# Optimization experiments

Hardware: AMD Instinct MI355X
Metric: run time of the kernel (lower is better)

## Reference

```python
import jax, jax.numpy as jnp
import numpy as np

BATCH = 1048576
IN_DIM = 64   # input_dim = A.shape[1]
OUT_DIM = 16  # output_dim = A.shape[0]


def setup_inputs() -> dict:
    key = jax.random.key(0)
    k1, k2, k3 = jax.random.split(key, 3)
    y = jax.random.normal(k1, (BATCH, IN_DIM), dtype=jnp.float32)
    A = jax.random.normal(k2, (OUT_DIM, IN_DIM), dtype=jnp.float32)
    b = jax.random.normal(k3, (BATCH, OUT_DIM), dtype=jnp.float32)
    return {"y": y, "A": A, "b": b}


def _block_matrix(A):
    # KKT block matrix [[2I, A^T], [A, 0]], shape (n+m, n+m); shared across batch.
    m, n = A.shape
    Id2 = 2.0 * jnp.eye(n, dtype=A.dtype)
    top = jnp.concatenate([Id2, A.T], axis=1)          # (n, n+m)
    bot = jnp.concatenate([A, jnp.zeros((m, m), A.dtype)], axis=1)  # (m, n+m)
    return jnp.concatenate([top, bot], axis=0)


def reference(y, A, b):
    # Solve block_matrix @ sol_i = [2*y_i; b_i] for all samples i in one batched solve
    # (original torch code loops torch.linalg.solve over the batch with the SAME matrix).
    n = A.shape[1]
    M = _block_matrix(A)                               # (n+m, n+m)
    rhs = jnp.concatenate([2.0 * y, b], axis=1)        # (batch, n+m)
    sol = jnp.linalg.solve(M, rhs.T).T                 # factorize once, all RHS at once
    y_star = sol[:, :n]
    return y_star
```

## Files before the change

kernel.cpp:

```cpp
#include <hip/hip_runtime.h>

#define BATCH   1048576
#define IN_DIM  64
#define OUT_DIM 16
#define NWAVE   4096
#define TPERW   16

typedef __attribute__((ext_vector_type(8))) short short8;
typedef __attribute__((ext_vector_type(4))) float f32x4;

__global__ __launch_bounds__(256) void precompute_kernel(
    const float* __restrict__ A, float* __restrict__ ws)
{
    __shared__ float sA[16][64];
    __shared__ float M[16][32];
    __shared__ float fac[16];
    __shared__ int piv;

    const int tid = threadIdx.x;

    for (int i = tid; i < 1024; i += 256) sA[i >> 6][i & 63] = A[i];
    __syncthreads();

    {
        const int i = tid >> 4, j = tid & 15;
        float s = 0.f;
        #pragma unroll
        for (int k = 0; k < 64; ++k) s = fmaf(sA[i][k], sA[j][k], s);
        M[i][j] = s;
        M[i][16 + j] = (i == j) ? 1.f : 0.f;
    }
    __syncthreads();

    for (int p = 0; p < 16; ++p) {
        if (tid == 0) {
            int best = p;
            float bv = fabsf(M[p][p]);
            for (int r = p + 1; r < 16; ++r) {
                float v = fabsf(M[r][p]);
                if (v > bv) { bv = v; best = r; }
            }
            piv = best;
        }
        __syncthreads();
        if (tid < 32) {
            const int pr = piv;
            if (pr != p) { float t = M[p][tid]; M[p][tid] = M[pr][tid]; M[pr][tid] = t; }
        }
        __syncthreads();
        const float pv = M[p][p];
        __syncthreads();
        if (tid < 32) M[p][tid] *= (1.0f / pv);
        __syncthreads();
        if (tid < 16) fac[tid] = M[tid][p];
        __syncthreads();
        for (int e = tid; e < 512; e += 256) {
            const int r = e >> 5, c = e & 31;
            if (r != p) M[r][c] = fmaf(-fac[r], M[p][c], M[r][c]);
        }
        __syncthreads();
    }

    for (int e = tid; e < 1024; e += 256) {
        const int k = e >> 4, i = e & 15;
        float s = 0.f;
        #pragma unroll
        for (int j = 0; j < 16; ++j) s = fmaf(M[i][16 + j], sA[j][k], s);
        ws[e] = s;
    }
}

__device__ __forceinline__ unsigned pack2(float a, float b, bool lo) {
    unsigned ua = __float_as_uint(a), ub = __float_as_uint(b);
    if (lo) {
        ua = __float_as_uint(a - __uint_as_float(ua & 0xFFFF0000u));
        ub = __float_as_uint(b - __uint_as_float(ub & 0xFFFF0000u));
    }
    return (ua >> 16) | (ub & 0xFFFF0000u);
}
__device__ __forceinline__ short8 pack8(float4 p, float4 q, bool lo) {
    union { short8 s; unsigned u[4]; } r;
    r.u[0] = pack2(p.x, p.y, lo);
    r.u[1] = pack2(p.z, p.w, lo);
    r.u[2] = pack2(q.x, q.y, lo);
    r.u[3] = pack2(q.z, q.w, lo);
    return r.s;
}

#define MF(a, bb, cc) __builtin_amdgcn_mfma_f32_16x16x32_bf16((a), (bb), (cc), 0, 0, 0)

__global__ __launch_bounds__(256, 4) void apply_kernel(
    const float* __restrict__ y, const float* __restrict__ b,
    const float* __restrict__ A, const float* __restrict__ ws,
    float* __restrict__ out)
{
    __shared__ float4 yT[4][16][17];
    __shared__ float4 bT[4][16][5];
    __shared__ float  tb[4][16 * 20];

    const int tid = threadIdx.x;
    const int wv = tid >> 6, l = tid & 63;
    const int lh = l & 15, lg = l >> 4;
    const int hf = lg & 1;
    const bool lolane = (lg >= 2);

    const float4* __restrict__ y4  = reinterpret_cast<const float4*>(y);
    const float4* __restrict__ b4  = reinterpret_cast<const float4*>(b);
    const float4* __restrict__ A4  = reinterpret_cast<const float4*>(A);
    const float4* __restrict__ Ct4 = reinterpret_cast<const float4*>(ws);
    float4* __restrict__ o4        = reinterpret_cast<float4*>(out);

    union { short8 s; unsigned u[4]; } zz;
    zz.u[0] = zz.u[1] = zz.u[2] = zz.u[3] = 0u;
    const short8 zero = zz.s;

    short8 B1_0, B1_1, B1_2, B1_3, B2_0, B2_1, B2_2, B2_3;
    {
        float4 a0, a1;
        a0 = A4[lh*16 + 0*4 + hf*2]; a1 = A4[lh*16 + 0*4 + hf*2 + 1];
        B1_0 = pack8(a0, a1, false); B2_0 = (lg < 2) ? pack8(a0, a1, true) : zero;
        a0 = A4[lh*16 + 1*4 + hf*2]; a1 = A4[lh*16 + 1*4 + hf*2 + 1];
        B1_1 = pack8(a0, a1, false); B2_1 = (lg < 2) ? pack8(a0, a1, true) : zero;
        a0 = A4[lh*16 + 2*4 + hf*2]; a1 = A4[lh*16 + 2*4 + hf*2 + 1];
        B1_2 = pack8(a0, a1, false); B2_2 = (lg < 2) ? pack8(a0, a1, true) : zero;
        a0 = A4[lh*16 + 3*4 + hf*2]; a1 = A4[lh*16 + 3*4 + hf*2 + 1];
        B1_3 = pack8(a0, a1, false); B2_3 = (lg < 2) ? pack8(a0, a1, true) : zero;
    }
    short8 C1_0, C1_1, C1_2, C1_3, C2_0, C2_1, C2_2, C2_3;
    {
        float4 c0, c1;
        #define LOADC(n) \
            c0 = Ct4[((n)*16+lh)*4 + hf*2]; c1 = Ct4[((n)*16+lh)*4 + hf*2 + 1]; \
            c0.x=-c0.x; c0.y=-c0.y; c0.z=-c0.z; c0.w=-c0.w; \
            c1.x=-c1.x; c1.y=-c1.y; c1.z=-c1.z; c1.w=-c1.w; \
            C1_##n = pack8(c0, c1, false); \
            C2_##n = (lg < 2) ? pack8(c0, c1, true) : zero;
        LOADC(0) LOADC(1) LOADC(2) LOADC(3)
        #undef LOADC
    }

    size_t tile = (size_t)blockIdx.x * 4 + wv;

    const float4* ysrc = y4 + tile * 256;
    float4 g0 = ysrc[l];
    float4 g1 = ysrc[64 + l];
    float4 g2 = ysrc[128 + l];
    float4 g3 = ysrc[192 + l];
    float4 gb = b4[tile * 64 + l];

    #pragma unroll 1
    for (int s = 0; s < TPERW; ++s) {
        yT[wv][0*4 + lg][lh] = g0;
        yT[wv][1*4 + lg][lh] = g1;
        yT[wv][2*4 + lg][lh] = g2;
        yT[wv][3*4 + lg][lh] = g3;
        bT[wv][l >> 2][l & 3] = gb;

        if (s + 1 < TPERW) {
            const float4* yn = y4 + (tile + NWAVE) * 256;
            g0 = yn[l];
            g1 = yn[64 + l];
            g2 = yn[128 + l];
            g3 = yn[192 + l];
            gb = b4[(tile + NWAVE) * 64 + l];
        }

        f32x4 acc = {0.f, 0.f, 0.f, 0.f};
        {
            short8 af;
            float4 f0, f1;
            f0 = yT[wv][lh][0*4 + hf*2]; f1 = yT[wv][lh][0*4 + hf*2 + 1];
            af = pack8(f0, f1, lolane);
            acc = MF(af, B1_0, acc); acc = MF(af, B2_0, acc);
            f0 = yT[wv][lh][1*4 + hf*2]; f1 = yT[wv][lh][1*4 + hf*2 + 1];
            af = pack8(f0, f1, lolane);
            acc = MF(af, B1_1, acc); acc = MF(af, B2_1, acc);
            f0 = yT[wv][lh][2*4 + hf*2]; f1 = yT[wv][lh][2*4 + hf*2 + 1];
            af = pack8(f0, f1, lolane);
            acc = MF(af, B1_2, acc); acc = MF(af, B2_2, acc);
            f0 = yT[wv][lh][3*4 + hf*2]; f1 = yT[wv][lh][3*4 + hf*2 + 1];
            af = pack8(f0, f1, lolane);
            acc = MF(af, B1_3, acc); acc = MF(af, B2_3, acc);
        }

        tb[wv][(4*lg + 0)*20 + lh] = acc[0];
        tb[wv][(4*lg + 1)*20 + lh] = acc[1];
        tb[wv][(4*lg + 2)*20 + lh] = acc[2];
        tb[wv][(4*lg + 3)*20 + lh] = acc[3];
        short8 TF;
        {
            float4 t0 = *reinterpret_cast<const float4*>(&tb[wv][lh*20 + hf*8]);
            float4 t1 = *reinterpret_cast<const float4*>(&tb[wv][lh*20 + hf*8 + 4]);
            const float4 bb0 = bT[wv][lh][hf*2];
            const float4 bb1 = bT[wv][lh][hf*2 + 1];
            t0.x -= bb0.x; t0.y -= bb0.y; t0.z -= bb0.z; t0.w -= bb0.w;
            t1.x -= bb1.x; t1.y -= bb1.y; t1.z -= bb1.z; t1.w -= bb1.w;
            TF = pack8(t0, t1, lolane);
        }

        float* yF = reinterpret_cast<float*>(&yT[wv][0][0]);
        #define STRIP(n) { \
            f32x4 x; \
            x[0] = yF[(4*lg + 0)*68 + (n)*16 + lh]; \
            x[1] = yF[(4*lg + 1)*68 + (n)*16 + lh]; \
            x[2] = yF[(4*lg + 2)*68 + (n)*16 + lh]; \
            x[3] = yF[(4*lg + 3)*68 + (n)*16 + lh]; \
            x = MF(TF, C1_##n, x); x = MF(TF, C2_##n, x); \
            yF[(4*lg + 0)*68 + (n)*16 + lh] = x[0]; \
            yF[(4*lg + 1)*68 + (n)*16 + lh] = x[1]; \
            yF[(4*lg + 2)*68 + (n)*16 + lh] = x[2]; \
            yF[(4*lg + 3)*68 + (n)*16 + lh] = x[3]; }
        STRIP(0) STRIP(1) STRIP(2) STRIP(3)
        #undef STRIP

        float4* odst = o4 + tile * 256;
        odst[l]       = yT[wv][0*4 + lg][lh];
        odst[64 + l]  = yT[wv][1*4 + lg][lh];
        odst[128 + l] = yT[wv][2*4 + lg][lh];
        odst[192 + l] = yT[wv][3*4 + lg][lh];

        tile += NWAVE;
    }
}

extern "C" void kernel_launch(void* const* d_in, const int* in_sizes, int n_in,
                              void* d_out, int out_size, void* d_ws, size_t ws_size,
                              hipStream_t stream) {
    const float* y = (const float*)d_in[0];
    const float* A = (const float*)d_in[1];
    const float* b = (const float*)d_in[2];
    float* out = (float*)d_out;
    float* ws  = (float*)d_ws;

    precompute_kernel<<<1, 256, 0, stream>>>(A, ws);
    apply_kernel<<<1024, 256, 0, stream>>>(y, b, A, ws, out);
}
```

Before: 142.1 us.

## Load b in accumulator layout, store output straight from MFMA registers, widen grid

The b tile is now loaded directly into the MFMA accumulator layout and subtracted in registers, which removes the bT shared staging buffer and its reads. Output values go from the second MFMA result straight to global memory instead of being written back to the yT shared buffer and then copied out. The grid grows from 1024 to 4096 blocks with 4 tiles per wave instead of 16, giving more parallelism and shorter prefetch loops. In exchange, the b loads and output stores become scalar strided accesses (16 contiguous floats per group) rather than float4 coalesced ones.

```diff
diff --git a/kernel.cpp b/kernel.cpp
--- a/kernel.cpp
+++ b/kernel.cpp
@@ -3,8 +3,9 @@
 #define BATCH   1048576
 #define IN_DIM  64
 #define OUT_DIM 16
-#define NWAVE   4096
-#define TPERW   16
+#define NBLK    4096
+#define NWTOT   16384
+#define TPERW   4
 
 typedef __attribute__((ext_vector_type(8))) short short8;
 typedef __attribute__((ext_vector_type(4))) float f32x4;
@@ -95,7 +96,6 @@
     float* __restrict__ out)
 {
     __shared__ float4 yT[4][16][17];
-    __shared__ float4 bT[4][16][5];
     __shared__ float  tb[4][16 * 20];
 
     const int tid = threadIdx.x;
@@ -105,10 +105,8 @@
     const bool lolane = (lg >= 2);
 
     const float4* __restrict__ y4  = reinterpret_cast<const float4*>(y);
-    const float4* __restrict__ b4  = reinterpret_cast<const float4*>(b);
     const float4* __restrict__ A4  = reinterpret_cast<const float4*>(A);
     const float4* __restrict__ Ct4 = reinterpret_cast<const float4*>(ws);
-    float4* __restrict__ o4        = reinterpret_cast<float4*>(out);
 
     union { short8 s; unsigned u[4]; } zz;
     zz.u[0] = zz.u[1] = zz.u[2] = zz.u[3] = 0u;
@@ -146,7 +144,11 @@
     float4 g1 = ysrc[64 + l];
     float4 g2 = ysrc[128 + l];
     float4 g3 = ysrc[192 + l];
-    float4 gb = b4[tile * 64 + l];
+    const float* bsrc = b + tile * 256;
+    float bc0 = bsrc[(4*lg + 0)*16 + lh];
+    float bc1 = bsrc[(4*lg + 1)*16 + lh];
+    float bc2 = bsrc[(4*lg + 2)*16 + lh];
+    float bc3 = bsrc[(4*lg + 3)*16 + lh];
 
     #pragma unroll 1
     for (int s = 0; s < TPERW; ++s) {
@@ -154,15 +156,19 @@
         yT[wv][1*4 + lg][lh] = g1;
         yT[wv][2*4 + lg][lh] = g2;
         yT[wv][3*4 + lg][lh] = g3;
-        bT[wv][l >> 2][l & 3] = gb;
+        const float tb0 = bc0, tb1 = bc1, tb2 = bc2, tb3 = bc3;
 
         if (s + 1 < TPERW) {
-            const float4* yn = y4 + (tile + NWAVE) * 256;
+            const float4* yn = y4 + (tile + NWTOT) * 256;
             g0 = yn[l];
             g1 = yn[64 + l];
             g2 = yn[128 + l];
             g3 = yn[192 + l];
-            gb = b4[(tile + NWAVE) * 64 + l];
+            const float* bn = b + (tile + NWTOT) * 256;
+            bc0 = bn[(4*lg + 0)*16 + lh];
+            bc1 = bn[(4*lg + 1)*16 + lh];
+            bc2 = bn[(4*lg + 2)*16 + lh];
+            bc3 = bn[(4*lg + 3)*16 + lh];
         }
 
         f32x4 acc = {0.f, 0.f, 0.f, 0.f};
@@ -182,6 +188,7 @@
             af = pack8(f0, f1, lolane);
             acc = MF(af, B1_3, acc); acc = MF(af, B2_3, acc);
         }
+        acc[0] -= tb0; acc[1] -= tb1; acc[2] -= tb2; acc[3] -= tb3;
 
         tb[wv][(4*lg + 0)*20 + lh] = acc[0];
         tb[wv][(4*lg + 1)*20 + lh] = acc[1];
@@ -189,16 +196,13 @@
         tb[wv][(4*lg + 3)*20 + lh] = acc[3];
         short8 TF;
         {
-            float4 t0 = *reinterpret_cast<const float4*>(&tb[wv][lh*20 + hf*8]);
-            float4 t1 = *reinterpret_cast<const float4*>(&tb[wv][lh*20 + hf*8 + 4]);
-            const float4 bb0 = bT[wv][lh][hf*2];
-            const float4 bb1 = bT[wv][lh][hf*2 + 1];
-            t0.x -= bb0.x; t0.y -= bb0.y; t0.z -= bb0.z; t0.w -= bb0.w;
-            t1.x -= bb1.x; t1.y -= bb1.y; t1.z -= bb1.z; t1.w -= bb1.w;
+            const float4 t0 = *reinterpret_cast<const float4*>(&tb[wv][lh*20 + hf*8]);
+            const float4 t1 = *reinterpret_cast<const float4*>(&tb[wv][lh*20 + hf*8 + 4]);
             TF = pack8(t0, t1, lolane);
         }
 
-        float* yF = reinterpret_cast<float*>(&yT[wv][0][0]);
+        const float* yF = reinterpret_cast<const float*>(&yT[wv][0][0]);
+        float* ob = out + tile * 1024;
         #define STRIP(n) { \
             f32x4 x; \
             x[0] = yF[(4*lg + 0)*68 + (n)*16 + lh]; \
@@ -206,20 +210,14 @@
             x[2] = yF[(4*lg + 2)*68 + (n)*16 + lh]; \
             x[3] = yF[(4*lg + 3)*68 + (n)*16 + lh]; \
             x = MF(TF, C1_##n, x); x = MF(TF, C2_##n, x); \
-            yF[(4*lg + 0)*68 + (n)*16 + lh] = x[0]; \
-            yF[(4*lg + 1)*68 + (n)*16 + lh] = x[1]; \
-            yF[(4*lg + 2)*68 + (n)*16 + lh] = x[2]; \
-            yF[(4*lg + 3)*68 + (n)*16 + lh] = x[3]; }
+            ob[(4*lg + 0)*64 + (n)*16 + lh] = x[0]; \
+            ob[(4*lg + 1)*64 + (n)*16 + lh] = x[1]; \
+            ob[(4*lg + 2)*64 + (n)*16 + lh] = x[2]; \
+            ob[(4*lg + 3)*64 + (n)*16 + lh] = x[3]; }
         STRIP(0) STRIP(1) STRIP(2) STRIP(3)
         #undef STRIP
 
-        float4* odst = o4 + tile * 256;
-        odst[l]       = yT[wv][0*4 + lg][lh];
-        odst[64 + l]  = yT[wv][1*4 + lg][lh];
-        odst[128 + l] = yT[wv][2*4 + lg][lh];
-        odst[192 + l] = yT[wv][3*4 + lg][lh];
-
-        tile += NWAVE;
+        tile += NWTOT;
     }
 }
 
@@ -233,5 +231,5 @@
     float* ws  = (float*)d_ws;
 
     precompute_kernel<<<1, 256, 0, stream>>>(A, ws);
-    apply_kernel<<<1024, 256, 0, stream>>>(y, b, A, ws, out);
-}
+    apply_kernel<<<NBLK, 256, 0, stream>>>(y, b, A, ws, out);
+}
```

Result: slower. 168.9 us (+18.9%).

## Swap MFMA operand order to transpose outputs and launch more blocks

Applied to the files above, without the earlier changes.

The MFMA A/B operands are swapped so the accumulator comes out transposed. That lets b be subtracted in registers, with b loaded in the matching lane order, and lets y be updated through float4 LDS accesses instead of scalar strided ones. The separate bT staging buffer is removed. The grid grows from 1024 to 4096 blocks with 4 tiles per wave instead of 16, which raises parallelism but shortens the per-wave prefetch pipeline.

```diff
diff --git a/kernel.cpp b/kernel.cpp
--- a/kernel.cpp
+++ b/kernel.cpp
@@ -3,8 +3,9 @@
 #define BATCH   1048576
 #define IN_DIM  64
 #define OUT_DIM 16
-#define NWAVE   4096
-#define TPERW   16
+#define NBLK    4096
+#define NWTOT   16384
+#define TPERW   4
 
 typedef __attribute__((ext_vector_type(8))) short short8;
 typedef __attribute__((ext_vector_type(4))) float f32x4;
@@ -95,8 +96,7 @@
     float* __restrict__ out)
 {
     __shared__ float4 yT[4][16][17];
-    __shared__ float4 bT[4][16][5];
-    __shared__ float  tb[4][16 * 20];
+    __shared__ float4 tb[4][16][5];
 
     const int tid = threadIdx.x;
     const int wv = tid >> 6, l = tid & 63;
@@ -146,7 +146,7 @@
     float4 g1 = ysrc[64 + l];
     float4 g2 = ysrc[128 + l];
     float4 g3 = ysrc[192 + l];
-    float4 gb = b4[tile * 64 + l];
+    float4 gb = b4[tile * 64 + lh * 4 + lg];
 
     #pragma unroll 1
     for (int s = 0; s < TPERW; ++s) {
@@ -154,15 +154,15 @@
         yT[wv][1*4 + lg][lh] = g1;
         yT[wv][2*4 + lg][lh] = g2;
         yT[wv][3*4 + lg][lh] = g3;
-        bT[wv][l >> 2][l & 3] = gb;
+        const float4 bv = gb;
 
         if (s + 1 < TPERW) {
-            const float4* yn = y4 + (tile + NWAVE) * 256;
+            const float4* yn = y4 + (tile + NWTOT) * 256;
             g0 = yn[l];
             g1 = yn[64 + l];
             g2 = yn[128 + l];
             g3 = yn[192 + l];
-            gb = b4[(tile + NWAVE) * 64 + l];
+            gb = b4[(tile + NWTOT) * 64 + lh * 4 + lg];
         }
 
         f32x4 acc = {0.f, 0.f, 0.f, 0.f};
@@ -171,45 +171,32 @@
             float4 f0, f1;
             f0 = yT[wv][lh][0*4 + hf*2]; f1 = yT[wv][lh][0*4 + hf*2 + 1];
             af = pack8(f0, f1, lolane);
-            acc = MF(af, B1_0, acc); acc = MF(af, B2_0, acc);
+            acc = MF(B1_0, af, acc); acc = MF(B2_0, af, acc);
             f0 = yT[wv][lh][1*4 + hf*2]; f1 = yT[wv][lh][1*4 + hf*2 + 1];
             af = pack8(f0, f1, lolane);
-            acc = MF(af, B1_1, acc); acc = MF(af, B2_1, acc);
+            acc = MF(B1_1, af, acc); acc = MF(B2_1, af, acc);
             f0 = yT[wv][lh][2*4 + hf*2]; f1 = yT[wv][lh][2*4 + hf*2 + 1];
             af = pack8(f0, f1, lolane);
-            acc = MF(af, B1_2, acc); acc = MF(af, B2_2, acc);
+            acc = MF(B1_2, af, acc); acc = MF(B2_2, af, acc);
             f0 = yT[wv][lh][3*4 + hf*2]; f1 = yT[wv][lh][3*4 + hf*2 + 1];
             af = pack8(f0, f1, lolane);
-            acc = MF(af, B1_3, acc); acc = MF(af, B2_3, acc);
-        }
-
-        tb[wv][(4*lg + 0)*20 + lh] = acc[0];
-        tb[wv][(4*lg + 1)*20 + lh] = acc[1];
-        tb[wv][(4*lg + 2)*20 + lh] = acc[2];
-        tb[wv][(4*lg + 3)*20 + lh] = acc[3];
+            acc = MF(B1_3, af, acc); acc = MF(B2_3, af, acc);
+        }
+        acc[0] -= bv.x; acc[1] -= bv.y; acc[2] -= bv.z; acc[3] -= bv.w;
+
+        tb[wv][lh][lg] = make_float4(acc[0], acc[1], acc[2], acc[3]);
         short8 TF;
         {
-            float4 t0 = *reinterpret_cast<const float4*>(&tb[wv][lh*20 + hf*8]);
-            float4 t1 = *reinterpret_cast<const float4*>(&tb[wv][lh*20 + hf*8 + 4]);
-            const float4 bb0 = bT[wv][lh][hf*2];
-            const float4 bb1 = bT[wv][lh][hf*2 + 1];
-            t0.x -= bb0.x; t0.y -= bb0.y; t0.z -= bb0.z; t0.w -= bb0.w;
-            t1.x -= bb1.x; t1.y -= bb1.y; t1.z -= bb1.z; t1.w -= bb1.w;
+            const float4 t0 = tb[wv][lh][2*hf];
+            const float4 t1 = tb[wv][lh][2*hf + 1];
             TF = pack8(t0, t1, lolane);
         }
 
-        float* yF = reinterpret_cast<float*>(&yT[wv][0][0]);
         #define STRIP(n) { \
-            f32x4 x; \
-            x[0] = yF[(4*lg + 0)*68 + (n)*16 + lh]; \
-            x[1] = yF[(4*lg + 1)*68 + (n)*16 + lh]; \
-            x[2] = yF[(4*lg + 2)*68 + (n)*16 + lh]; \
-            x[3] = yF[(4*lg + 3)*68 + (n)*16 + lh]; \
-            x = MF(TF, C1_##n, x); x = MF(TF, C2_##n, x); \
-            yF[(4*lg + 0)*68 + (n)*16 + lh] = x[0]; \
-            yF[(4*lg + 1)*68 + (n)*16 + lh] = x[1]; \
-            yF[(4*lg + 2)*68 + (n)*16 + lh] = x[2]; \
-            yF[(4*lg + 3)*68 + (n)*16 + lh] = x[3]; }
+            const float4 sd = yT[wv][lh][(n)*4 + lg]; \
+            f32x4 x = {sd.x, sd.y, sd.z, sd.w}; \
+            x = MF(C1_##n, TF, x); x = MF(C2_##n, TF, x); \
+            yT[wv][lh][(n)*4 + lg] = make_float4(x[0], x[1], x[2], x[3]); }
         STRIP(0) STRIP(1) STRIP(2) STRIP(3)
         #undef STRIP
 
@@ -219,7 +206,7 @@
         odst[128 + l] = yT[wv][2*4 + lg][lh];
         odst[192 + l] = yT[wv][3*4 + lg][lh];
 
-        tile += NWAVE;
+        tile += NWTOT;
     }
 }
 
@@ -233,5 +220,5 @@
     float* ws  = (float*)d_ws;
 
     precompute_kernel<<<1, 256, 0, stream>>>(A, ws);
-    apply_kernel<<<1024, 256, 0, stream>>>(y, b, A, ws, out);
-}
+    apply_kernel<<<NBLK, 256, 0, stream>>>(y, b, A, ws, out);
+}
```

Measured after the change: 141.3 us. About the same (-0.5%).
